# Kernel tuning notes

Hardware: AMD Instinct MI355X
Metric: run time of the kernel (lower is better)

The kernel has to match this reference:

```python
import jax, jax.numpy as jnp
import numpy as np

INPUT, HIDDEN, CLASSES = 4096, 4096, 1000


def setup_inputs() -> dict:
    key = jax.random.key(0)
    kx, kw1, kb1, kw2, kb2 = jax.random.split(key, 5)
    return {
        "x": jax.random.normal(kx, (8192, INPUT), dtype=jnp.float32),
        "fc1_weight": jax.random.normal(kw1, (HIDDEN, INPUT), dtype=jnp.float32),
        "fc1_bias": jax.random.normal(kb1, (HIDDEN,), dtype=jnp.float32),
        "fc2_weight": jax.random.normal(kw2, (CLASSES, HIDDEN), dtype=jnp.float32),
        "fc2_bias": jax.random.normal(kb2, (CLASSES,), dtype=jnp.float32),
    }


def reference(x, fc1_weight, fc1_bias, fc2_weight, fc2_bias):
    # x: [B, INPUT] (module flattens; already flat here)
    hidden = jnp.einsum("bi,hi->bh", x, fc1_weight) + fc1_bias  # [B, H]
    activated = jax.nn.relu(hidden)
    logits = jnp.einsum("bh,ch->bc", activated, fc2_weight) + fc2_bias  # [B, C]
    return jax.nn.softmax(logits, axis=-1)
```

## Files before the change

### kernel.cpp

```cpp
#include <hip/hip_runtime.h>
#include <hip/hip_fp16.h>
#include <stdint.h>

typedef __attribute__((ext_vector_type(8))) _Float16 f16x8;
typedef __attribute__((ext_vector_type(4))) _Float16 f16x4;
typedef __attribute__((ext_vector_type(4))) float f32x4;

__device__ __forceinline__ void split4(const f32x4 v, f16x4 &h, f16x4 &l) {
    #pragma unroll
    for (int i = 0; i < 4; ++i) {
        float a = v[i];
        _Float16 hh = (_Float16)a;
        h[i] = hh;
        l[i] = (_Float16)(a - (float)hh);
    }
}

__global__ __launch_bounds__(256)
void split_rows(const float* __restrict__ src, _Float16* __restrict__ h,
                _Float16* __restrict__ l, int srcRows, long long total4)
{
    const long long stride = (long long)gridDim.x * blockDim.x;
    for (long long i = (long long)blockIdx.x * blockDim.x + threadIdx.x; i < total4; i += stride) {
        const long long e = i << 2;
        const int row = (int)(e >> 12);
        f16x4 hv = {}, lv = {};
        if (row < srcRows) {
            f32x4 v = *(const f32x4*)(src + e);
            split4(v, hv, lv);
        }
        *(f16x4*)(h + e) = hv;
        *(f16x4*)(l + e) = lv;
    }
}


#define BARRIER() __builtin_amdgcn_s_barrier()
#define SB0()     __builtin_amdgcn_sched_barrier(0)
#define MFMA16    __builtin_amdgcn_mfma_f32_16x16x32_f16

template<int N> __device__ __forceinline__ void VMCNT() {
    asm volatile("s_waitcnt vmcnt(%0)" :: "n"(N) : "memory");
    __builtin_amdgcn_sched_barrier(0);
}

__device__ __forceinline__ void gload16(const _Float16* g, _Float16* l) {
    __builtin_amdgcn_global_load_lds(
        (const __attribute__((address_space(1))) void*)g,
        (__attribute__((address_space(3))) void*)l, 16, 0, 0);
}

template<int MI, bool SPLITOUT, bool CHUNKSWZ>
__global__ __launch_bounds__(512, 2)
void gemm3_v5(const _Float16* __restrict__ Agh, const _Float16* __restrict__ Agl,
              const _Float16* __restrict__ Bgh, const _Float16* __restrict__ Bgl,
              const float* __restrict__ bias,
              _Float16* __restrict__ Oh, _Float16* __restrict__ Ol,
              float* __restrict__ Of, int ldo, int Nstore,
              int K, int nBM)
{
    extern __shared__ _Float16 lds[];
    constexpr int WROWS = MI * 16;
    constexpr int BM    = MI * 32;
    constexpr int CHA   = MI * 2;
    constexpr int PW    = (2*CHA + 32) / 8;
    constexpr int NA    = PW - 4;
    constexpr int ALO   = CHA * 512;
    constexpr int BHO   = 2 * CHA * 512;
    constexpr int BUFS  = 2*CHA*512 + 16384;

    const int tid  = threadIdx.x;
    const int lane = tid & 63;
    const int wave = tid >> 6;
    const int wm = wave >> 2;
    const int wn = wave & 3;
    const int fr = lane & 15;
    const int fg = lane >> 4;

    int bm, bn;
    const int orig = blockIdx.x;
    if (CHUNKSWZ) {
        bm = ((orig & 7) << 2) | ((orig >> 3) & 3);
        bn = orig >> 5;
    } else {
        const int cpx  = gridDim.x >> 3;
        const int swzb = (orig & 7) * cpx + (orig >> 3);
        bm = swzb % nBM;
        bn = swzb / nBM;
    }
    const int m0 = bm * BM;
    const int n0 = bn * 256;

    const _Float16* gptr[8];
    int loff[8];
    #pragma unroll
    for (int i = 0; i < PW; ++i) {
        int p, q;
        if (i < NA) {
            const int j = wave * NA + i;
            p = j / CHA; q = j % CHA;
        } else {
            const int ni = i - NA;
            q = ni + (wave & 3) * 4;
            p = 2 + (wave >> 2);
        }
        const int row = q*16 + (lane >> 2);
        const int gc  = (lane & 3) ^ ((row >> 1) & 3);
        const _Float16* plane = (p == 0) ? Agh : (p == 1) ? Agl : (p == 2) ? Bgh : Bgl;
        const size_t grow = (size_t)((p < 2) ? m0 : n0) + row;
        gptr[i] = plane + grow * (size_t)K + gc * 8;
        loff[i] = ((p < 2) ? p * ALO : BHO + (p - 2) * 8192) + q * 512;
    }

    const int swz8 = (fg ^ ((fr >> 1) & 3)) * 8;
    int aoff[MI], boff[4];
    #pragma unroll
    for (int mi = 0; mi < MI; ++mi) aoff[mi] = (wm*WROWS + mi*16 + fr)*32 + swz8;
    #pragma unroll
    for (int ni = 0; ni < 4; ++ni)  boff[ni] = BHO + (wn*64 + ni*16 + fr)*32 + swz8;

    f32x4 acc[MI][4] = {};

    #pragma unroll
    for (int i = 0; i < PW; ++i) { gload16(gptr[i], &lds[loff[i]]); gptr[i] += 32; }
    VMCNT<2>(); BARRIER(); SB0();

#define DO_HALF(NIa, NIb, IB, IE, STG)                                        \
    do {                                                                      \
        const f16x8 bha = *(const f16x8*)&lds[bb + boff[NIa]];                \
        const f16x8 bla = *(const f16x8*)&lds[bb + 8192 + boff[NIa]];         \
        const f16x8 bhb = *(const f16x8*)&lds[bb + boff[NIb]];                \
        const f16x8 blb = *(const f16x8*)&lds[bb + 8192 + boff[NIb]];         \
        if (STG) {                                                            \
            _Pragma("unroll")                                                 \
            for (int i = (IB); i < (IE); ++i) {                               \
                gload16(gptr[i], &lds[nb + loff[i]]); gptr[i] += 32;          \
            }                                                                 \
        }                                                                     \
        SB0();                                                                \
        __builtin_amdgcn_s_setprio(1);                                        \
        _Pragma("unroll")                                                     \
        for (int mi = 0; mi < MI; ++mi) {                                     \
            const f16x8 ah = *(const f16x8*)&lds[bb + aoff[mi]];              \
            const f16x8 al = *(const f16x8*)&lds[bb + ALO + aoff[mi]];        \
            acc[mi][NIa] = MFMA16(ah, bha, acc[mi][NIa], 0, 0, 0);            \
            acc[mi][NIa] = MFMA16(ah, bla, acc[mi][NIa], 0, 0, 0);            \
            acc[mi][NIa] = MFMA16(al, bha, acc[mi][NIa], 0, 0, 0);            \
            acc[mi][NIb] = MFMA16(ah, bhb, acc[mi][NIb], 0, 0, 0);            \
            acc[mi][NIb] = MFMA16(ah, blb, acc[mi][NIb], 0, 0, 0);            \
            acc[mi][NIb] = MFMA16(al, bhb, acc[mi][NIb], 0, 0, 0);            \
        }                                                                     \
        __builtin_amdgcn_s_setprio(0);                                        \
    } while (0)

    const int NT = K >> 5;
    int bb = 0;
    for (int t = 0; t < NT - 1; ++t) {
        const int nb = BUFS - bb;
        DO_HALF(0, 1, 0, NA + 2, true);
        VMCNT<NA + 2>(); BARRIER(); SB0();
        DO_HALF(2, 3, NA + 2, PW, true);
        VMCNT<2>(); BARRIER(); SB0();
        bb = nb;
    }
    {
        const int nb = 0; (void)nb;
        DO_HALF(0, 1, 0, 0, false);
        VMCNT<0>(); BARRIER(); SB0();
        DO_HALF(2, 3, 0, 0, false);
    }
#undef DO_HALF

    #pragma unroll
    for (int ni = 0; ni < 4; ++ni) {
        const int n = n0 + wn*64 + ni*16 + fr;
        if (!SPLITOUT && n >= Nstore) continue;
        const float bv = bias[n];
        #pragma unroll
        for (int mi = 0; mi < MI; ++mi) {
            #pragma unroll
            for (int j = 0; j < 4; ++j) {
                const int m = m0 + wm*WROWS + mi*16 + fg*4 + j;
                float v = acc[mi][ni][j] + bv;
                if (SPLITOUT) {
                    v = fmaxf(v, 0.f);
                    const _Float16 hh = (_Float16)v;
                    Oh[(size_t)m * ldo + n] = hh;
                    Ol[(size_t)m * ldo + n] = (_Float16)(v - (float)hh);
                } else {
                    Of[(size_t)m * ldo + n] = v;
                }
            }
        }
    }
}

#define TILE_M 128
#define TILE_N 128
#define TILE_K 32
#define LDSK   40

template<bool RELU, bool NGUARD>
__global__ __launch_bounds__(256, 2)
void gemm_split3(const float* __restrict__ A, const float* __restrict__ B,
                 const float* __restrict__ bias, float* __restrict__ C,
                 int K, int ldc, int Nreal)
{
    __shared__ _Float16 Ah[TILE_M][LDSK];
    __shared__ _Float16 Al[TILE_M][LDSK];
    __shared__ _Float16 Bh[TILE_N][LDSK];
    __shared__ _Float16 Bl[TILE_N][LDSK];

    const int tid  = threadIdx.x;
    const int lane = tid & 63;
    const int wave = tid >> 6;
    const int wr   = wave >> 1;
    const int wc   = wave & 1;
    const int m0   = blockIdx.x * TILE_M;
    const int n0   = blockIdx.y * TILE_N;
    const int srow = tid >> 3;
    const int scol = (tid & 7) << 2;
    const int fr = lane & 15;
    const int fg = lane >> 4;

    f32x4 acc[4][4] = {};

    for (int kt = 0; kt < K; kt += TILE_K) {
        __syncthreads();
        #pragma unroll
        for (int p = 0; p < 4; ++p) {
            const int row = srow + p * 32;
            f32x4 v = *(const f32x4*)(A + (size_t)(m0 + row) * K + kt + scol);
            f16x4 hv, lv;
            split4(v, hv, lv);
            *(f16x4*)&Ah[row][scol] = hv;
            *(f16x4*)&Al[row][scol] = lv;
        }
        #pragma unroll
        for (int p = 0; p < 4; ++p) {
            const int row = srow + p * 32;
            f32x4 v = {0.f, 0.f, 0.f, 0.f};
            if (!NGUARD || (n0 + row) < Nreal)
                v = *(const f32x4*)(B + (size_t)(n0 + row) * K + kt + scol);
            f16x4 hv, lv;
            split4(v, hv, lv);
            *(f16x4*)&Bh[row][scol] = hv;
            *(f16x4*)&Bl[row][scol] = lv;
        }
        __syncthreads();

        f16x8 ah[4], al[4];
        #pragma unroll
        for (int mi = 0; mi < 4; ++mi) {
            const int r = wr * 64 + mi * 16 + fr;
            ah[mi] = *(const f16x8*)&Ah[r][fg * 8];
            al[mi] = *(const f16x8*)&Al[r][fg * 8];
        }
        #pragma unroll
        for (int ni = 0; ni < 4; ++ni) {
            const int r = wc * 64 + ni * 16 + fr;
            const f16x8 bh = *(const f16x8*)&Bh[r][fg * 8];
            const f16x8 bl = *(const f16x8*)&Bl[r][fg * 8];
            #pragma unroll
            for (int mi = 0; mi < 4; ++mi) {
                acc[mi][ni] = __builtin_amdgcn_mfma_f32_16x16x32_f16(ah[mi], bh, acc[mi][ni], 0, 0, 0);
                acc[mi][ni] = __builtin_amdgcn_mfma_f32_16x16x32_f16(ah[mi], bl, acc[mi][ni], 0, 0, 0);
                acc[mi][ni] = __builtin_amdgcn_mfma_f32_16x16x32_f16(al[mi], bh, acc[mi][ni], 0, 0, 0);
            }
        }
    }

    #pragma unroll
    for (int ni = 0; ni < 4; ++ni) {
        const int n = n0 + wc * 64 + ni * 16 + fr;
        if (NGUARD && n >= Nreal) continue;
        const float bv = bias[n];
        #pragma unroll
        for (int mi = 0; mi < 4; ++mi) {
            #pragma unroll
            for (int j = 0; j < 4; ++j) {
                const int m = m0 + wr * 64 + mi * 16 + fg * 4 + j;
                float val = acc[mi][ni][j] + bv;
                if (RELU) val = fmaxf(val, 0.f);
                C[(size_t)m * ldc + n] = val;
            }
        }
    }
}

__global__ __launch_bounds__(256)
void softmax_rows(float* __restrict__ out, int rows, int cols)
{
    const int lane = threadIdx.x & 63;
    const int row  = blockIdx.x * 4 + (threadIdx.x >> 6);
    if (row >= rows) return;
    float* p = out + (size_t)row * cols;

    float v[16];
    float mx = -3.4e38f;
    #pragma unroll
    for (int j = 0; j < 16; ++j) {
        const int c = lane + j * 64;
        v[j] = (c < cols) ? p[c] : -3.4e38f;
        mx = fmaxf(mx, v[j]);
    }
    #pragma unroll
    for (int off = 32; off > 0; off >>= 1)
        mx = fmaxf(mx, __shfl_xor(mx, off));

    float s = 0.f;
    #pragma unroll
    for (int j = 0; j < 16; ++j) {
        const int c = lane + j * 64;
        const float e = (c < cols) ? __expf(v[j] - mx) : 0.f;
        v[j] = e;
        s += e;
    }
    #pragma unroll
    for (int off = 32; off > 0; off >>= 1)
        s += __shfl_xor(s, off);

    const float inv = 1.f / s;
    #pragma unroll
    for (int j = 0; j < 16; ++j) {
        const int c = lane + j * 64;
        if (c < cols) p[c] = v[j] * inv;
    }
}

extern "C" void kernel_launch(void* const* d_in, const int* in_sizes, int n_in,
                              void* d_out, int out_size, void* d_ws, size_t ws_size,
                              hipStream_t stream)
{
    const float* x  = (const float*)d_in[0];
    const float* w1 = (const float*)d_in[1];
    const float* b1 = (const float*)d_in[2];
    const float* w2 = (const float*)d_in[3];
    const float* b2 = (const float*)d_in[4];
    float* out = (float*)d_out;

    const size_t SZ_X  = (size_t)8192 * 4096 * 2;
    const size_t SZ_W1 = (size_t)4096 * 4096 * 2;
    const size_t SZ_W2 = (size_t)1024 * 4096 * 2;

    size_t off = 0;
    auto take = [&](size_t b) { size_t o = off; off += (b + 255) & ~(size_t)255; return o; };
    const size_t o_xh  = take(SZ_X),  o_xl  = take(SZ_X);
    const size_t o_w1h = take(SZ_W1), o_w1l = take(SZ_W1);
    const size_t o_w2h = take(SZ_W2), o_w2l = take(SZ_W2);
    const size_t o_ah  = take(SZ_X),  o_al  = take(SZ_X);
    const size_t need = off;

    bool attr_ok =
        (hipFuncSetAttribute((const void*)gemm3_v5<8, true, true>,
                             hipFuncAttributeMaxDynamicSharedMemorySize, 131072) == hipSuccess) &&
        (hipFuncSetAttribute((const void*)gemm3_v5<4, false, false>,
                             hipFuncAttributeMaxDynamicSharedMemorySize, 131072) == hipSuccess);

    const dim3 blk256(256, 1, 1), blk512(512, 1, 1);

    if (attr_ok && ws_size >= need) {
        char* w = (char*)d_ws;
        _Float16 *xh  = (_Float16*)(w + o_xh),  *xl  = (_Float16*)(w + o_xl);
        _Float16 *w1h = (_Float16*)(w + o_w1h), *w1l = (_Float16*)(w + o_w1l);
        _Float16 *w2h = (_Float16*)(w + o_w2h), *w2l = (_Float16*)(w + o_w2l);
        _Float16 *ath = (_Float16*)(w + o_ah),  *atl = (_Float16*)(w + o_al);

        hipLaunchKernelGGL(split_rows, dim3(2048), blk256, 0, stream, x,  xh,  xl,  8192, (long long)8192 * 1024);
        hipLaunchKernelGGL(split_rows, dim3(2048), blk256, 0, stream, w1, w1h, w1l, 4096, (long long)4096 * 1024);
        hipLaunchKernelGGL(split_rows, dim3(1024), blk256, 0, stream, w2, w2h, w2l, 1000, (long long)1024 * 1024);

        hipLaunchKernelGGL((gemm3_v5<8, true, true>), dim3(512), blk512, 131072, stream,
                           xh, xl, w1h, w1l, b1, ath, atl, (float*)nullptr, 4096, 4096, 4096, 32);
        hipLaunchKernelGGL((gemm3_v5<4, false, false>), dim3(256), blk512, 98304, stream,
                           ath, atl, w2h, w2l, b2, (_Float16*)nullptr, (_Float16*)nullptr,
                           out, 1000, 1000, 4096, 64);
        hipLaunchKernelGGL(softmax_rows, dim3(2048), blk256, 0, stream, out, 8192, 1000);
    } else {
        float* act = (float*)d_ws;
        hipLaunchKernelGGL((gemm_split3<true, false>), dim3(64, 32), blk256, 0, stream,
                           x, w1, b1, act, 4096, 4096, 4096);
        hipLaunchKernelGGL((gemm_split3<false, true>), dim3(64, 8), blk256, 0, stream,
                           act, w2, b2, out, 4096, 1000, 1000);
        hipLaunchKernelGGL(softmax_rows, dim3(2048), blk256, 0, stream, out, 8192, 1000);
    }
}
```

Baseline: 969.8 us.

## Switch split-fp16 GEMM to 32x32x16 MFMA tiles with reorganized prefetch halves

Replaces the 16x16x32 MFMA fragments with 32x32x16 MFMAs, so each wave holds 32x32 accumulator blocks and loads B fragments once per K-tile instead of per half. The pipelined global-to-LDS loads are regrouped: A rows are split by M-half so the first compute half only waits on its own A rows, and B loads move to the first half. The goal is fewer LDS fragment reads per FLOP and higher MFMA throughput. The trade-offs are more accumulator registers (16 floats per tile) and a different output scatter pattern.

```diff
diff --git a/kernel.cpp b/kernel.cpp
--- a/kernel.cpp
+++ b/kernel.cpp
@@ -2,9 +2,10 @@
 #include <hip/hip_fp16.h>
 #include <stdint.h>
 
-typedef __attribute__((ext_vector_type(8))) _Float16 f16x8;
-typedef __attribute__((ext_vector_type(4))) _Float16 f16x4;
-typedef __attribute__((ext_vector_type(4))) float f32x4;
+typedef __attribute__((ext_vector_type(8)))  _Float16 f16x8;
+typedef __attribute__((ext_vector_type(4)))  _Float16 f16x4;
+typedef __attribute__((ext_vector_type(4)))  float    f32x4;
+typedef __attribute__((ext_vector_type(16))) float    f32x16;
 
 __device__ __forceinline__ void split4(const f32x4 v, f16x4 &h, f16x4 &l) {
     #pragma unroll
@@ -37,7 +38,7 @@
 
 #define BARRIER() __builtin_amdgcn_s_barrier()
 #define SB0()     __builtin_amdgcn_sched_barrier(0)
-#define MFMA16    __builtin_amdgcn_mfma_f32_16x16x32_f16
+#define MFMA32    __builtin_amdgcn_mfma_f32_32x32x16_f16
 
 template<int N> __device__ __forceinline__ void VMCNT() {
     asm volatile("s_waitcnt vmcnt(%0)" :: "n"(N) : "memory");
@@ -52,7 +53,7 @@
 
 template<int MI, bool SPLITOUT, bool CHUNKSWZ>
 __global__ __launch_bounds__(512, 2)
-void gemm3_v5(const _Float16* __restrict__ Agh, const _Float16* __restrict__ Agl,
+void gemm3_v6(const _Float16* __restrict__ Agh, const _Float16* __restrict__ Agl,
               const _Float16* __restrict__ Bgh, const _Float16* __restrict__ Bgl,
               const float* __restrict__ bias,
               _Float16* __restrict__ Oh, _Float16* __restrict__ Ol,
@@ -62,9 +63,12 @@
     extern __shared__ _Float16 lds[];
     constexpr int WROWS = MI * 16;
     constexpr int BM    = MI * 32;
+    constexpr int MB    = MI / 2;
+    constexpr int MBH   = MB / 2;
     constexpr int CHA   = MI * 2;
     constexpr int PW    = (2*CHA + 32) / 8;
-    constexpr int NA    = PW - 4;
+    constexpr int H2    = CHA / 8;
+    constexpr int H1    = PW - H2;
     constexpr int ALO   = CHA * 512;
     constexpr int BHO   = 2 * CHA * 512;
     constexpr int BUFS  = 2*CHA*512 + 16384;
@@ -72,10 +76,10 @@
     const int tid  = threadIdx.x;
     const int lane = tid & 63;
     const int wave = tid >> 6;
-    const int wm = wave >> 2;
-    const int wn = wave & 3;
-    const int fr = lane & 15;
-    const int fg = lane >> 4;
+    const int wm  = wave >> 2;
+    const int wn  = wave & 3;
+    const int l31 = lane & 31;
+    const int lhi = lane >> 5;
 
     int bm, bn;
     const int orig = blockIdx.x;
@@ -96,12 +100,17 @@
     #pragma unroll
     for (int i = 0; i < PW; ++i) {
         int p, q;
-        if (i < NA) {
-            const int j = wave * NA + i;
-            p = j / CHA; q = j % CHA;
+        if (i < H2 || i >= H1) {
+            const bool hi = (i >= H1);
+            const int  s  = hi ? (i - H1) : i;
+            const int  j  = wave * H2 + s;
+            p = j / (CHA / 2);
+            const int v   = j % (CHA / 2);
+            const int wmq = v / (MI / 2);
+            const int wi  = v % (MI / 2);
+            q = wmq * MI + (hi ? MI / 2 : 0) + wi;
         } else {
-            const int ni = i - NA;
-            q = ni + (wave & 3) * 4;
+            q = (i - H2) + (wave & 3) * 4;
             p = 2 + (wave >> 2);
         }
         const int row = q*16 + (lane >> 2);
@@ -112,76 +121,100 @@
         loff[i] = ((p < 2) ? p * ALO : BHO + (p - 2) * 8192) + q * 512;
     }
 
-    const int swz8 = (fg ^ ((fr >> 1) & 3)) * 8;
-    int aoff[MI], boff[4];
-    #pragma unroll
-    for (int mi = 0; mi < MI; ++mi) aoff[mi] = (wm*WROWS + mi*16 + fr)*32 + swz8;
-    #pragma unroll
-    for (int ni = 0; ni < 4; ++ni)  boff[ni] = BHO + (wn*64 + ni*16 + fr)*32 + swz8;
-
-    f32x4 acc[MI][4] = {};
+    const int kxor = (l31 >> 1) & 3;
+    int aoff[MB][2], boff[2][2];
+    #pragma unroll
+    for (int mb = 0; mb < MB; ++mb)
+        #pragma unroll
+        for (int kh = 0; kh < 2; ++kh)
+            aoff[mb][kh] = (wm*WROWS + mb*32 + l31)*32 + ((kh*2 + lhi) ^ kxor)*8;
+    #pragma unroll
+    for (int nb = 0; nb < 2; ++nb)
+        #pragma unroll
+        for (int kh = 0; kh < 2; ++kh)
+            boff[nb][kh] = BHO + (wn*64 + nb*32 + l31)*32 + ((kh*2 + lhi) ^ kxor)*8;
+
+    f32x16 acc[MB][2] = {};
 
     #pragma unroll
     for (int i = 0; i < PW; ++i) { gload16(gptr[i], &lds[loff[i]]); gptr[i] += 32; }
-    VMCNT<2>(); BARRIER(); SB0();
-
-#define DO_HALF(NIa, NIb, IB, IE, STG)                                        \
+    VMCNT<H2>(); BARRIER(); SB0();
+
+#define DO_HALF(MBB, IB, IE)                                                  \
     do {                                                                      \
-        const f16x8 bha = *(const f16x8*)&lds[bb + boff[NIa]];                \
-        const f16x8 bla = *(const f16x8*)&lds[bb + 8192 + boff[NIa]];         \
-        const f16x8 bhb = *(const f16x8*)&lds[bb + boff[NIb]];                \
-        const f16x8 blb = *(const f16x8*)&lds[bb + 8192 + boff[NIb]];         \
-        if (STG) {                                                            \
-            _Pragma("unroll")                                                 \
-            for (int i = (IB); i < (IE); ++i) {                               \
-                gload16(gptr[i], &lds[nb + loff[i]]); gptr[i] += 32;          \
-            }                                                                 \
+        _Pragma("unroll")                                                     \
+        for (int i = (IB); i < (IE); ++i) {                                   \
+            gload16(gptr[i], &lds[nbuf + loff[i]]); gptr[i] += 32;            \
         }                                                                     \
         SB0();                                                                \
-        __builtin_amdgcn_s_setprio(1);                                        \
         _Pragma("unroll")                                                     \
-        for (int mi = 0; mi < MI; ++mi) {                                     \
-            const f16x8 ah = *(const f16x8*)&lds[bb + aoff[mi]];              \
-            const f16x8 al = *(const f16x8*)&lds[bb + ALO + aoff[mi]];        \
-            acc[mi][NIa] = MFMA16(ah, bha, acc[mi][NIa], 0, 0, 0);            \
-            acc[mi][NIa] = MFMA16(ah, bla, acc[mi][NIa], 0, 0, 0);            \
-            acc[mi][NIa] = MFMA16(al, bha, acc[mi][NIa], 0, 0, 0);            \
-            acc[mi][NIb] = MFMA16(ah, bhb, acc[mi][NIb], 0, 0, 0);            \
-            acc[mi][NIb] = MFMA16(ah, blb, acc[mi][NIb], 0, 0, 0);            \
-            acc[mi][NIb] = MFMA16(al, bhb, acc[mi][NIb], 0, 0, 0);            \
+        for (int kh = 0; kh < 2; ++kh) {                                      \
+            f16x8 ah[MBH], al[MBH];                                           \
+            _Pragma("unroll")                                                 \
+            for (int m2 = 0; m2 < MBH; ++m2) {                                \
+                ah[m2] = *(const f16x8*)&lds[bb + aoff[(MBB) + m2][kh]];      \
+                al[m2] = *(const f16x8*)&lds[bb + ALO + aoff[(MBB) + m2][kh]];\
+            }                                                                 \
+            __builtin_amdgcn_s_setprio(1);                                    \
+            _Pragma("unroll")                                                 \
+            for (int m2 = 0; m2 < MBH; ++m2) {                                \
+                _Pragma("unroll")                                             \
+                for (int n2 = 0; n2 < 2; ++n2) {                              \
+                    acc[(MBB)+m2][n2] = MFMA32(ah[m2], bh[n2][kh], acc[(MBB)+m2][n2], 0, 0, 0); \
+                    acc[(MBB)+m2][n2] = MFMA32(ah[m2], bl[n2][kh], acc[(MBB)+m2][n2], 0, 0, 0); \
+                    acc[(MBB)+m2][n2] = MFMA32(al[m2], bh[n2][kh], acc[(MBB)+m2][n2], 0, 0, 0); \
+                }                                                             \
+            }                                                                 \
+            __builtin_amdgcn_s_setprio(0);                                    \
         }                                                                     \
-        __builtin_amdgcn_s_setprio(0);                                        \
     } while (0)
 
     const int NT = K >> 5;
     int bb = 0;
     for (int t = 0; t < NT - 1; ++t) {
-        const int nb = BUFS - bb;
-        DO_HALF(0, 1, 0, NA + 2, true);
-        VMCNT<NA + 2>(); BARRIER(); SB0();
-        DO_HALF(2, 3, NA + 2, PW, true);
-        VMCNT<2>(); BARRIER(); SB0();
-        bb = nb;
+        const int nbuf = BUFS - bb;
+        f16x8 bh[2][2], bl[2][2];
+        #pragma unroll
+        for (int nb = 0; nb < 2; ++nb)
+            #pragma unroll
+            for (int kh = 0; kh < 2; ++kh) {
+                bh[nb][kh] = *(const f16x8*)&lds[bb + boff[nb][kh]];
+                bl[nb][kh] = *(const f16x8*)&lds[bb + 8192 + boff[nb][kh]];
+            }
+        DO_HALF(0, 0, H1);
+        VMCNT<H1>(); BARRIER(); SB0();
+        DO_HALF(MBH, H1, PW);
+        VMCNT<H2>(); BARRIER(); SB0();
+        bb = nbuf;
     }
     {
-        const int nb = 0; (void)nb;
-        DO_HALF(0, 1, 0, 0, false);
+        const int nbuf = bb;
+        f16x8 bh[2][2], bl[2][2];
+        #pragma unroll
+        for (int nb = 0; nb < 2; ++nb)
+            #pragma unroll
+            for (int kh = 0; kh < 2; ++kh) {
+                bh[nb][kh] = *(const f16x8*)&lds[bb + boff[nb][kh]];
+                bl[nb][kh] = *(const f16x8*)&lds[bb + 8192 + boff[nb][kh]];
+            }
+        DO_HALF(0, 0, 0);
         VMCNT<0>(); BARRIER(); SB0();
-        DO_HALF(2, 3, 0, 0, false);
+        DO_HALF(MBH, 0, 0);
+        (void)nbuf;
     }
 #undef DO_HALF
 
     #pragma unroll
-    for (int ni = 0; ni < 4; ++ni) {
-        const int n = n0 + wn*64 + ni*16 + fr;
+    for (int nb = 0; nb < 2; ++nb) {
+        const int n = n0 + wn*64 + nb*32 + l31;
         if (!SPLITOUT && n >= Nstore) continue;
         const float bv = bias[n];
         #pragma unroll
-        for (int mi = 0; mi < MI; ++mi) {
+        for (int mb = 0; mb < MB; ++mb) {
             #pragma unroll
-            for (int j = 0; j < 4; ++j) {
-                const int m = m0 + wm*WROWS + mi*16 + fg*4 + j;
-                float v = acc[mi][ni][j] + bv;
+            for (int r = 0; r < 16; ++r) {
+                const int m = m0 + wm*WROWS + mb*32 + (r & 3) + 8*(r >> 2) + 4*lhi;
+                float v = acc[mb][nb][r] + bv;
                 if (SPLITOUT) {
                     v = fmaxf(v, 0.f);
                     const _Float16 hh = (_Float16)v;
@@ -352,9 +385,9 @@
     const size_t need = off;
 
     bool attr_ok =
-        (hipFuncSetAttribute((const void*)gemm3_v5<8, true, true>,
+        (hipFuncSetAttribute((const void*)gemm3_v6<8, true, true>,
                              hipFuncAttributeMaxDynamicSharedMemorySize, 131072) == hipSuccess) &&
-        (hipFuncSetAttribute((const void*)gemm3_v5<4, false, false>,
+        (hipFuncSetAttribute((const void*)gemm3_v6<4, false, false>,
                              hipFuncAttributeMaxDynamicSharedMemorySize, 131072) == hipSuccess);
 
     const dim3 blk256(256, 1, 1), blk512(512, 1, 1);
@@ -370,9 +403,9 @@
         hipLaunchKernelGGL(split_rows, dim3(2048), blk256, 0, stream, w1, w1h, w1l, 4096, (long long)4096 * 1024);
         hipLaunchKernelGGL(split_rows, dim3(1024), blk256, 0, stream, w2, w2h, w2l, 1000, (long long)1024 * 1024);
 
-        hipLaunchKernelGGL((gemm3_v5<8, true, true>), dim3(512), blk512, 131072, stream,
+        hipLaunchKernelGGL((gemm3_v6<8, true, true>), dim3(512), blk512, 131072, stream,
                            xh, xl, w1h, w1l, b1, ath, atl, (float*)nullptr, 4096, 4096, 4096, 32);
-        hipLaunchKernelGGL((gemm3_v5<4, false, false>), dim3(256), blk512, 98304, stream,
+        hipLaunchKernelGGL((gemm3_v6<4, false, false>), dim3(256), blk512, 98304, stream,
                            ath, atl, w2h, w2l, b2, (_Float16*)nullptr, (_Float16*)nullptr,
                            out, 1000, 1000, 4096, 64);
         hipLaunchKernelGGL(softmax_rows, dim3(2048), blk256, 0, stream, out, 8192, 1000);
```

After: 1.033 ms. 6.5% more time.
